# Performance work log

Hardware: AMD Instinct MI355X
Metric: run time of the kernel (lower is better)

## Reference

```python
import jax, jax.numpy as jnp
import numpy as np

N, S, Z, H, K, DEG = 8192, 4, 64, 128, 4, 16
E = N * DEG


def setup_inputs() -> dict:
    key = jax.random.key(0)
    ks = jax.random.split(key, 9)
    g = lambda k, shape, scale=1.0: jax.random.normal(k, shape, dtype=jnp.float32) * scale
    return dict(
        zIG=g(ks[0], (N, S, Z)),                         # node intention features
        xt_enc=g(ks[1], (N, S, H)),                      # encoded actions per node
        Ws=g(ks[2], (K, H, Z), 1.0 / np.sqrt(Z)),        # attn_s[k] weights (no bias)
        Wd=g(ks[3], (K, H, Z), 1.0 / np.sqrt(Z)),        # attn_d[k] weights
        F2_w1=g(ks[4], (H, 2 * H), 1.0 / np.sqrt(2 * H)),
        F2_w2=g(ks[5], (H, H), 1.0 / np.sqrt(H)),
        F1_w1=g(ks[6], (H, K * H), 1.0 / np.sqrt(K * H)),
        F1_w2=g(ks[7], (H, H), 1.0 / np.sqrt(H)),
        src=jax.random.randint(ks[8], (E,), 0, N),       # random source per edge
        dst=jnp.repeat(jnp.arange(N), DEG),              # regular graph: DEG in-edges per node, grouped
    )


def reference(zIG, xt_enc, Ws, Wd, F2_w1, F2_w2, F1_w1, F1_w2, src, dst):
    n, s, h = xt_enc.shape
    k = Ws.shape[0]
    deg = src.shape[0] // n

    # ---- edge_attention: eIG[e,s,k] = leaky_relu(sum_h (Ws_k z_src)*(Wd_k z_dst)) ----
    zs, zd = zIG[src], zIG[dst]                          # [E,S,Z] irregular gathers
    scores = []
    for kk in range(k):                                  # k is small & structural
        a_s = zs @ Ws[kk].T                              # [E,S,H]
        a_d = zd @ Wd[kk].T                              # [E,S,H]
        scores.append(jax.nn.leaky_relu((a_s * a_d).sum(-1)))  # [E,S]
    eIG = jnp.stack(scores, axis=-1)                     # [E,S,K]

    # ---- message_func: dA = F2(cat(xt_src, xt_dst)) ----
    msg_in = jnp.concatenate([xt_enc[src], xt_enc[dst]], axis=-1)   # [E,S,2H]
    dA = jax.nn.relu(msg_in @ F2_w1.T) @ F2_w2.T                    # [E,S,H]

    # ---- reduce_func: softmax over neighbor mailbox (dim=1), weighted mean ----
    # dst is grouped with constant degree, so the DGL mailbox is a reshape.
    alpha = jax.nn.softmax(eIG.reshape(n, deg, s, k), axis=1)       # [N,D,S,K]
    mail = dA.reshape(n, deg, s, h)                                 # [N,D,S,H]
    res = jnp.einsum('ndsk,ndsh->nskh', alpha, mail) / deg          # mean over D
    res = res.reshape(n, s, k * h)                                  # cat over k (k-major)
    deltax = jax.nn.relu(res @ F1_w1.T) @ F1_w2.T                   # [N,S,H]
    return deltax, alpha
```

## Files before the change

### kernel.cpp

```cpp
#include <hip/hip_runtime.h>
#include <hip/hip_bf16.h>

typedef unsigned short u16;
typedef unsigned int u32;
using ushort8 = __attribute__((ext_vector_type(8))) unsigned short;
using short8  = __attribute__((ext_vector_type(8))) short;
using f32x4   = __attribute__((ext_vector_type(4))) float;

__device__ __forceinline__ float bf2f(u16 v) {
  union { u32 u; float f; } x; x.u = ((u32)v) << 16; return x.f;
}
__device__ __forceinline__ float u2f(u32 u) {
  union { u32 u; float f; } x; x.u = u; return x.f;
}
__device__ __forceinline__ u16 f2bf(float f) {
  union { u32 u; float f; } x; x.f = f;
  u32 r = x.u + 0x7FFFu + ((x.u >> 16) & 1u);
  return (u16)(r >> 16);
}
__device__ __forceinline__ u32 pack2bf(float lo, float hi) {
  return (u32)f2bf(lo) | ((u32)f2bf(hi) << 16);
}
__device__ __forceinline__ float dot4(float4 a, float4 b) {
  return a.x * b.x + a.y * b.y + a.z * b.z + a.w * b.w;
}
__device__ __forceinline__ void split8(const float* ap, short8& hi, short8& lo) {
  float4 a0 = *(const float4*)ap, a1 = *(const float4*)(ap + 4);
  float e[8] = {a0.x, a0.y, a0.z, a0.w, a1.x, a1.y, a1.z, a1.w};
  u16 h[8], l[8];
  #pragma unroll
  for (int j = 0; j < 8; ++j) {
    u32 b = __float_as_uint(e[j]);
    h[j] = (u16)(b >> 16);
    l[j] = f2bf(e[j] - u2f(b & 0xffff0000u));
  }
  hi = *(short8*)h; lo = *(short8*)l;
}
__device__ __forceinline__ void stage_w(const float* g, int stride, int c, u16* Wl, int t) {
  int row = t >> 1, half = t & 1;
  const float4* gp = (const float4*)(g + (size_t)row * stride + c * 64 + half * 32);
  ushort8* d = (ushort8*)(Wl + row * 72 + half * 32);
  #pragma unroll
  for (int i = 0; i < 4; ++i) {
    float4 a = gp[2 * i], b = gp[2 * i + 1];
    ushort8 o;
    o[0] = f2bf(a.x); o[1] = f2bf(a.y); o[2] = f2bf(a.z); o[3] = f2bf(a.w);
    o[4] = f2bf(b.x); o[5] = f2bf(b.y); o[6] = f2bf(b.z); o[7] = f2bf(b.w);
    d[i] = o;
  }
}
__device__ __forceinline__ void stage_w512(const float* g, int stride, int c, u16* Wl, int t) {
  int row = t >> 2, q = t & 3;
  const float4* gp = (const float4*)(g + (size_t)row * stride + c * 64 + q * 16);
  ushort8* d = (ushort8*)(Wl + row * 72 + q * 16);
  #pragma unroll
  for (int i = 0; i < 2; ++i) {
    float4 a = gp[2 * i], b = gp[2 * i + 1];
    ushort8 o;
    o[0] = f2bf(a.x); o[1] = f2bf(a.y); o[2] = f2bf(a.z); o[3] = f2bf(a.w);
    o[4] = f2bf(b.x); o[5] = f2bf(b.y); o[6] = f2bf(b.z); o[7] = f2bf(b.w);
    d[i] = o;
  }
}

__global__ __launch_bounds__(256) void k_prep(const float* __restrict__ Ws,
                                              const float* __restrict__ Wd,
                                              const float* __restrict__ F1w1,
                                              const float* __restrict__ F2w2,
                                              u16* __restrict__ Bh, u16* __restrict__ Bl,
                                              float* __restrict__ WW2) {
  if (blockIdx.x < 64) {
    int t = blockIdx.x * 256 + threadIdx.x;
    int k = t >> 12, z1 = (t >> 6) & 63, z2 = t & 63;
    const float* wsp = Ws + k * 8192 + z1;
    const float* wdp = Wd + k * 8192 + z2;
    float acc = 0.f;
    #pragma unroll 8
    for (int h = 0; h < 128; ++h) acc += wsp[h * 64] * wdp[h * 64];
    u32 b = __float_as_uint(acc);
    Bh[(k * 64 + z1) * 64 + z2] = (u16)(b >> 16);
    Bl[(k * 64 + z1) * 64 + z2] = f2bf(acc - u2f(b & 0xffff0000u));
  } else {
    int id = (blockIdx.x - 64) * 256 + threadIdx.x;
    int ho = id >> 9, kk = (id >> 7) & 3, hi = id & 127;
    const float* wa = F1w1 + ho * 512 + kk * 128;
    const float* wb = F2w2 + hi;
    float acc = 0.f;
    #pragma unroll 8
    for (int j = 0; j < 128; ++j) acc += wa[j] * wb[j * 128];
    WW2[ho * 512 + kk * 128 + hi] = acc * 0.0625f;
  }
}

__global__ __launch_bounds__(256) void k_tduv(const float* __restrict__ zIG,
                                              const u16* __restrict__ Bh_g,
                                              const u16* __restrict__ Bl_g,
                                              const float* __restrict__ xt,
                                              const float* __restrict__ W1,
                                              float* __restrict__ td,
                                              u16* __restrict__ u, u16* __restrict__ v) {
  __shared__ __align__(16) u16 SM[128 * 72];
  int t = threadIdx.x, lane = t & 63, w = t >> 6;
  int l15 = lane & 15, kc = lane >> 4;
  if (blockIdx.x < 1024) {
    u16* Bh = SM;
    u16* Bl = SM + 64 * 72;
    int cq = blockIdx.x & 3;
    size_t rowbase = (size_t)(blockIdx.x >> 2) * 128 + w * 32;
    {
      int row = t >> 2, q = t & 3;
      const ushort8* gh = (const ushort8*)(Bh_g + (cq * 64 + row) * 64 + q * 16);
      const ushort8* gl = (const ushort8*)(Bl_g + (cq * 64 + row) * 64 + q * 16);
      ushort8* dh = (ushort8*)(Bh + row * 72 + q * 16);
      ushort8* dl = (ushort8*)(Bl + row * 72 + q * 16);
      dh[0] = gh[0]; dh[1] = gh[1];
      dl[0] = gl[0]; dl[1] = gl[1];
    }
    __syncthreads();
    f32x4 acc[2][4];
    #pragma unroll
    for (int mt = 0; mt < 2; ++mt)
      #pragma unroll
      for (int nt = 0; nt < 4; ++nt) acc[mt][nt] = (f32x4){0.f, 0.f, 0.f, 0.f};
    #pragma unroll
    for (int ks = 0; ks < 2; ++ks) {
      short8 ah[2], al[2];
      #pragma unroll
      for (int mt = 0; mt < 2; ++mt)
        split8(zIG + (rowbase + mt * 16 + l15) * 64 + ks * 32 + kc * 8, ah[mt], al[mt]);
      #pragma unroll
      for (int nt = 0; nt < 4; ++nt) {
        int bo = (nt * 16 + l15) * 72 + ks * 32 + kc * 8;
        short8 bh = *(const short8*)&Bh[bo];
        short8 bl = *(const short8*)&Bl[bo];
        #pragma unroll
        for (int mt = 0; mt < 2; ++mt) {
          acc[mt][nt] = __builtin_amdgcn_mfma_f32_16x16x32_bf16(ah[mt], bh, acc[mt][nt], 0, 0, 0);
          acc[mt][nt] = __builtin_amdgcn_mfma_f32_16x16x32_bf16(al[mt], bh, acc[mt][nt], 0, 0, 0);
          acc[mt][nt] = __builtin_amdgcn_mfma_f32_16x16x32_bf16(ah[mt], bl, acc[mt][nt], 0, 0, 0);
        }
      }
    }
    #pragma unroll
    for (int mt = 0; mt < 2; ++mt)
      #pragma unroll
      for (int nt = 0; nt < 4; ++nt)
        #pragma unroll
        for (int j = 0; j < 4; ++j)
          td[(rowbase + mt * 16 + kc * 4 + j) * 256 + cq * 64 + nt * 16 + l15] =
              acc[mt][nt][j];
  } else {
    u16* Wl = SM;
    int bid2 = blockIdx.x - 1024;
    int sel = bid2 >> 8;
    size_t rowbase = (size_t)(bid2 & 255) * 128 + w * 32;
    const float* Wbase = W1 + sel * 128;
    f32x4 acc[2][8];
    #pragma unroll
    for (int mt = 0; mt < 2; ++mt)
      #pragma unroll
      for (int nt = 0; nt < 8; ++nt) acc[mt][nt] = (f32x4){0.f, 0.f, 0.f, 0.f};
    for (int c = 0; c < 2; ++c) {
      __syncthreads();
      stage_w(Wbase, 256, c, Wl, t);
      __syncthreads();
      #pragma unroll
      for (int ks = 0; ks < 2; ++ks) {
        short8 af[2];
        #pragma unroll
        for (int mt = 0; mt < 2; ++mt) {
          const float* ap = xt + (rowbase + mt * 16 + l15) * 128 + c * 64 + ks * 32 + kc * 8;
          float4 a0 = *(const float4*)ap, a1 = *(const float4*)(ap + 4);
          u16 tmp[8] = {f2bf(a0.x), f2bf(a0.y), f2bf(a0.z), f2bf(a0.w),
                        f2bf(a1.x), f2bf(a1.y), f2bf(a1.z), f2bf(a1.w)};
          af[mt] = *(short8*)tmp;
        }
        #pragma unroll
        for (int nt = 0; nt < 8; ++nt) {
          short8 bw = *(const short8*)&Wl[(nt * 16 + l15) * 72 + ks * 32 + kc * 8];
          #pragma unroll
          for (int mt = 0; mt < 2; ++mt)
            acc[mt][nt] = __builtin_amdgcn_mfma_f32_16x16x32_bf16(af[mt], bw, acc[mt][nt], 0, 0, 0);
        }
      }
    }
    u16* dstp = sel ? v : u;
    #pragma unroll
    for (int mt = 0; mt < 2; ++mt)
      #pragma unroll
      for (int nt = 0; nt < 8; ++nt)
        #pragma unroll
        for (int j = 0; j < 4; ++j)
          dstp[(rowbase + mt * 16 + kc * 4 + j) * 128 + nt * 16 + l15] =
              f2bf(acc[mt][nt][j]);
  }
}

__global__ __launch_bounds__(256) void k_edge(
    const float* __restrict__ zIG, const int* __restrict__ src,
    const float* __restrict__ td, float* __restrict__ out) {
  __shared__ int srcIdx[16];
  __shared__ float tds[16 * 68];
  __shared__ float s17[16 * 17];

  int t = threadIdx.x, n = blockIdx.x;
  if (t < 16) srcIdx[t] = src[n * 16 + t];
  {
    int r = t >> 4, cc = t & 15;
    *(float4*)&tds[r * 68 + cc * 4] = ((const float4*)(td + (size_t)n * 1024))[r * 16 + cc];
  }
  __syncthreads();
  {
    int d = t >> 4, s = (t >> 2) & 3, k = t & 3;
    int sn = srcIdx[d];
    const float4* zp = (const float4*)(zIG + (size_t)sn * 256 + s * 64);
    int base = s * 4;
    float p0 = 0.f, p1 = 0.f, p2 = 0.f, p3 = 0.f;
    #pragma unroll
    for (int i = 0; i < 4; ++i) {
      float4 zv = zp[i * 4 + k];
      int o = i * 16 + k * 4;
      p0 += dot4(zv, *(const float4*)&tds[(base + 0) * 68 + o]);
      p1 += dot4(zv, *(const float4*)&tds[(base + 1) * 68 + o]);
      p2 += dot4(zv, *(const float4*)&tds[(base + 2) * 68 + o]);
      p3 += dot4(zv, *(const float4*)&tds[(base + 3) * 68 + o]);
    }
    p0 += __shfl_xor(p0, 1); p1 += __shfl_xor(p1, 1);
    p2 += __shfl_xor(p2, 1); p3 += __shfl_xor(p3, 1);
    p0 += __shfl_xor(p0, 2); p1 += __shfl_xor(p1, 2);
    p2 += __shfl_xor(p2, 2); p3 += __shfl_xor(p3, 2);
    float acc = (k == 0) ? p0 : (k == 1) ? p1 : (k == 2) ? p2 : p3;
    s17[d * 17 + base + k] = acc > 0.f ? acc : 0.01f * acc;
  }
  __syncthreads();
  {
    int d = t >> 4, sk = t & 15;
    float mx = -3.4e38f;
    #pragma unroll
    for (int dd = 0; dd < 16; ++dd) mx = fmaxf(mx, s17[dd * 17 + sk]);
    float sum = 0.f, eown = 0.f;
    #pragma unroll
    for (int dd = 0; dd < 16; ++dd) {
      float e = __expf(s17[dd * 17 + sk] - mx);
      sum += e;
      if (dd == d) eown = e;
    }
    out[4194304u + (unsigned)n * 256 + t] = eown / sum;
  }
}

__global__ __launch_bounds__(256) void k_mail(
    const int* __restrict__ src, const float* __restrict__ alpha_g,
    const u16* __restrict__ uW, const u16* __restrict__ vW, u16* __restrict__ m_ws) {
  __shared__ int srcIdx[16];
  __shared__ float al[256];
  int t = threadIdx.x, n = blockIdx.x;
  if (t < 16) srcIdx[t] = src[n * 16 + t];
  al[t] = alpha_g[(size_t)n * 256 + t];
  __syncthreads();
  int hp = t & 63, s = t >> 6;
  u32 vbits = *(const u32*)(vW + (size_t)n * 512 + s * 128 + hp * 2);
  float v_lo = u2f(vbits << 16), v_hi = u2f(vbits & 0xffff0000u);
  const u32* up = (const u32*)uW;
  float m0l = 0.f, m0h = 0.f, m1l = 0.f, m1h = 0.f;
  float m2l = 0.f, m2h = 0.f, m3l = 0.f, m3h = 0.f;
  #pragma unroll
  for (int d = 0; d < 16; ++d) {
    u32 ub = up[(size_t)srcIdx[d] * 256 + s * 64 + hp];
    float r_lo = fmaxf(u2f(ub << 16) + v_lo, 0.f);
    float r_hi = fmaxf(u2f(ub & 0xffff0000u) + v_hi, 0.f);
    float4 a = *(const float4*)&al[d * 16 + s * 4];
    m0l += a.x * r_lo; m0h += a.x * r_hi;
    m1l += a.y * r_lo; m1h += a.y * r_hi;
    m2l += a.z * r_lo; m2h += a.z * r_hi;
    m3l += a.w * r_lo; m3h += a.w * r_hi;
  }
  u32* mp = (u32*)(m_ws + (size_t)n * 2048);
  mp[(s * 4 + 0) * 64 + hp] = pack2bf(m0l, m0h);
  mp[(s * 4 + 1) * 64 + hp] = pack2bf(m1l, m1h);
  mp[(s * 4 + 2) * 64 + hp] = pack2bf(m2l, m2h);
  mp[(s * 4 + 3) * 64 + hp] = pack2bf(m3l, m3h);
}

__global__ __launch_bounds__(512) void k_fg(const u16* __restrict__ A,
                                            const float* __restrict__ WF,
                                            const float* __restrict__ WG,
                                            float* __restrict__ out) {
  __shared__ u16 Wl[128 * 72];
  __shared__ u16 hidl[128 * 136];
  int t = threadIdx.x, lane = t & 63, w = t >> 6;
  size_t rowbase = (size_t)blockIdx.x * 128 + w * 16;
  int l15 = lane & 15, kc = lane >> 4;
  f32x4 acc[8];
  #pragma unroll
  for (int nt = 0; nt < 8; ++nt) acc[nt] = (f32x4){0.f, 0.f, 0.f, 0.f};
  for (int c = 0; c < 8; ++c) {
    __syncthreads();
    stage_w512(WF, 512, c, Wl, t);
    __syncthreads();
    #pragma unroll
    for (int ks = 0; ks < 2; ++ks) {
      short8 af = *(const short8*)(A + (rowbase + l15) * 512 + c * 64 + ks * 32 + kc * 8);
      #pragma unroll
      for (int nt = 0; nt < 8; ++nt) {
        short8 bf = *(const short8*)&Wl[(nt * 16 + l15) * 72 + ks * 32 + kc * 8];
        acc[nt] = __builtin_amdgcn_mfma_f32_16x16x32_bf16(af, bf, acc[nt], 0, 0, 0);
      }
    }
  }
  #pragma unroll
  for (int nt = 0; nt < 8; ++nt)
    #pragma unroll
    for (int j = 0; j < 4; ++j)
      hidl[(w * 16 + kc * 4 + j) * 136 + nt * 16 + l15] = f2bf(fmaxf(acc[nt][j], 0.f));
  f32x4 acc2[8];
  #pragma unroll
  for (int nt = 0; nt < 8; ++nt) acc2[nt] = (f32x4){0.f, 0.f, 0.f, 0.f};
  for (int c = 0; c < 2; ++c) {
    __syncthreads();
    stage_w512(WG, 128, c, Wl, t);
    __syncthreads();
    #pragma unroll
    for (int ks = 0; ks < 2; ++ks) {
      short8 af = *(const short8*)&hidl[(w * 16 + l15) * 136 + c * 64 + ks * 32 + kc * 8];
      #pragma unroll
      for (int nt = 0; nt < 8; ++nt) {
        short8 bf = *(const short8*)&Wl[(nt * 16 + l15) * 72 + ks * 32 + kc * 8];
        acc2[nt] = __builtin_amdgcn_mfma_f32_16x16x32_bf16(af, bf, acc2[nt], 0, 0, 0);
      }
    }
  }
  #pragma unroll
  for (int nt = 0; nt < 8; ++nt)
    #pragma unroll
    for (int j = 0; j < 4; ++j)
      out[(rowbase + kc * 4 + j) * 128 + nt * 16 + l15] = acc2[nt][j];
}

extern "C" void kernel_launch(void* const* d_in, const int* in_sizes, int n_in,
                              void* d_out, int out_size, void* d_ws, size_t ws_size,
                              hipStream_t stream) {
  const float* zIG  = (const float*)d_in[0];
  const float* xt   = (const float*)d_in[1];
  const float* Ws   = (const float*)d_in[2];
  const float* Wd   = (const float*)d_in[3];
  const float* F2w1 = (const float*)d_in[4];
  const float* F2w2 = (const float*)d_in[5];
  const float* F1w1 = (const float*)d_in[6];
  const float* F1w2 = (const float*)d_in[7];
  const int* src    = (const int*)d_in[8];
  float* out = (float*)d_out;

  char* ws = (char*)d_ws;
  u16* Bh    = (u16*)ws;
  u16* Bl    = Bh + 16384;
  float* td  = (float*)(ws + 65536);
  u16* u     = (u16*)(ws + 65536 + 33554432);
  u16* v     = u + 4194304;
  float* WW2 = (float*)(ws + 50397184);
  u16* m     = (u16*)(ws + 50659328);

  k_prep <<<320,  256, 0, stream>>>(Ws, Wd, F1w1, F2w2, Bh, Bl, WW2);
  k_tduv <<<1536, 256, 0, stream>>>(zIG, Bh, Bl, xt, F2w1, td, u, v);
  k_edge <<<8192, 256, 0, stream>>>(zIG, src, td, out);
  k_mail <<<8192, 256, 0, stream>>>(src, out + 4194304, u, v, m);
  k_fg   <<<256,  512, 0, stream>>>(m, WW2, F1w2, out);
}
```

Before: 104.1 us.

## Fuse edge-score softmax and mailbox aggregation into one kernel with prefetched gathers

Merges k_edge and k_mail into a single per-node kernel. The softmax weights now stay in shared memory instead of being written out and read back from global memory, and one launch is removed. The 16 irregular u-row gathers and the v load are issued early, before the score computation, so their latency overlaps with it. In exchange each thread holds 16 more registers, which may lower occupancy.

```diff
diff --git a/kernel.cpp b/kernel.cpp
--- a/kernel.cpp
+++ b/kernel.cpp
@@ -196,12 +196,14 @@
   }
 }
 
-__global__ __launch_bounds__(256) void k_edge(
+__global__ __launch_bounds__(256) void k_score(
     const float* __restrict__ zIG, const int* __restrict__ src,
-    const float* __restrict__ td, float* __restrict__ out) {
+    const float* __restrict__ td, const u16* __restrict__ uW, const u16* __restrict__ vW,
+    float* __restrict__ out, u16* __restrict__ m_ws) {
   __shared__ int srcIdx[16];
   __shared__ float tds[16 * 68];
   __shared__ float s17[16 * 17];
+  __shared__ float a20[16 * 20];
 
   int t = threadIdx.x, n = blockIdx.x;
   if (t < 16) srcIdx[t] = src[n * 16 + t];
@@ -210,6 +212,13 @@
     *(float4*)&tds[r * 68 + cc * 4] = ((const float4*)(td + (size_t)n * 1024))[r * 16 + cc];
   }
   __syncthreads();
+  int hp = t & 63, sD = t >> 6;
+  const u32* up = (const u32*)uW;
+  u32 upre[16];
+  #pragma unroll
+  for (int dd = 0; dd < 16; ++dd)
+    upre[dd] = up[(size_t)srcIdx[dd] * 256 + sD * 64 + hp];
+  u32 vbits = *(const u32*)(vW + (size_t)n * 512 + sD * 128 + hp * 2);
   {
     int d = t >> 4, s = (t >> 2) & 3, k = t & 3;
     int sn = srcIdx[d];
@@ -245,41 +254,32 @@
       sum += e;
       if (dd == d) eown = e;
     }
-    out[4194304u + (unsigned)n * 256 + t] = eown / sum;
-  }
-}
-
-__global__ __launch_bounds__(256) void k_mail(
-    const int* __restrict__ src, const float* __restrict__ alpha_g,
-    const u16* __restrict__ uW, const u16* __restrict__ vW, u16* __restrict__ m_ws) {
-  __shared__ int srcIdx[16];
-  __shared__ float al[256];
-  int t = threadIdx.x, n = blockIdx.x;
-  if (t < 16) srcIdx[t] = src[n * 16 + t];
-  al[t] = alpha_g[(size_t)n * 256 + t];
+    float a = eown / sum;
+    a20[d * 20 + sk] = a;
+    out[4194304u + (unsigned)n * 256 + t] = a;
+  }
   __syncthreads();
-  int hp = t & 63, s = t >> 6;
-  u32 vbits = *(const u32*)(vW + (size_t)n * 512 + s * 128 + hp * 2);
-  float v_lo = u2f(vbits << 16), v_hi = u2f(vbits & 0xffff0000u);
-  const u32* up = (const u32*)uW;
-  float m0l = 0.f, m0h = 0.f, m1l = 0.f, m1h = 0.f;
-  float m2l = 0.f, m2h = 0.f, m3l = 0.f, m3h = 0.f;
-  #pragma unroll
-  for (int d = 0; d < 16; ++d) {
-    u32 ub = up[(size_t)srcIdx[d] * 256 + s * 64 + hp];
-    float r_lo = fmaxf(u2f(ub << 16) + v_lo, 0.f);
-    float r_hi = fmaxf(u2f(ub & 0xffff0000u) + v_hi, 0.f);
-    float4 a = *(const float4*)&al[d * 16 + s * 4];
-    m0l += a.x * r_lo; m0h += a.x * r_hi;
-    m1l += a.y * r_lo; m1h += a.y * r_hi;
-    m2l += a.z * r_lo; m2h += a.z * r_hi;
-    m3l += a.w * r_lo; m3h += a.w * r_hi;
-  }
-  u32* mp = (u32*)(m_ws + (size_t)n * 2048);
-  mp[(s * 4 + 0) * 64 + hp] = pack2bf(m0l, m0h);
-  mp[(s * 4 + 1) * 64 + hp] = pack2bf(m1l, m1h);
-  mp[(s * 4 + 2) * 64 + hp] = pack2bf(m2l, m2h);
-  mp[(s * 4 + 3) * 64 + hp] = pack2bf(m3l, m3h);
+  {
+    float v_lo = u2f(vbits << 16), v_hi = u2f(vbits & 0xffff0000u);
+    float m0l = 0.f, m0h = 0.f, m1l = 0.f, m1h = 0.f;
+    float m2l = 0.f, m2h = 0.f, m3l = 0.f, m3h = 0.f;
+    #pragma unroll
+    for (int dd = 0; dd < 16; ++dd) {
+      u32 ub = upre[dd];
+      float r_lo = fmaxf(u2f(ub << 16) + v_lo, 0.f);
+      float r_hi = fmaxf(u2f(ub & 0xffff0000u) + v_hi, 0.f);
+      float4 a = *(const float4*)&a20[dd * 20 + sD * 4];
+      m0l += a.x * r_lo; m0h += a.x * r_hi;
+      m1l += a.y * r_lo; m1h += a.y * r_hi;
+      m2l += a.z * r_lo; m2h += a.z * r_hi;
+      m3l += a.w * r_lo; m3h += a.w * r_hi;
+    }
+    u32* mp = (u32*)(m_ws + (size_t)n * 2048);
+    mp[(sD * 4 + 0) * 64 + hp] = pack2bf(m0l, m0h);
+    mp[(sD * 4 + 1) * 64 + hp] = pack2bf(m1l, m1h);
+    mp[(sD * 4 + 2) * 64 + hp] = pack2bf(m2l, m2h);
+    mp[(sD * 4 + 3) * 64 + hp] = pack2bf(m3l, m3h);
+  }
 }
 
 __global__ __launch_bounds__(512) void k_fg(const u16* __restrict__ A,
@@ -362,7 +362,6 @@
 
   k_prep <<<320,  256, 0, stream>>>(Ws, Wd, F1w1, F2w2, Bh, Bl, WW2);
   k_tduv <<<1536, 256, 0, stream>>>(zIG, Bh, Bl, xt, F2w1, td, u, v);
-  k_edge <<<8192, 256, 0, stream>>>(zIG, src, td, out);
-  k_mail <<<8192, 256, 0, stream>>>(src, out + 4194304, u, v, m);
+  k_score<<<8192, 256, 0, stream>>>(zIG, src, td, u, v, out, m);
   k_fg   <<<256,  512, 0, stream>>>(m, WW2, F1w2, out);
 }
```

New measurement: 100.7 us, median of 2. -3.2%, faster.
